# Kernel tuning notes

Hardware: AMD Instinct MI355X
Metric: run time of the kernel (lower is better)

## Reference

```python
import jax, jax.numpy as jnp
import numpy as np

NUM_LABELS = 64  # number of distinct label ids (0 = background, unchanged)


def setup_inputs() -> dict:
    key = jax.random.key(0)
    k1, k2, k3 = jax.random.split(key, 3)
    shape = (2, 192, 256, 256)
    texturized = jax.random.normal(k1, shape, dtype=jnp.float32)
    label_map = jax.random.randint(k2, shape, 0, NUM_LABELS, dtype=jnp.int32)
    # one Uniform(0, intensity) draw per label, mirroring self.intensity() per loop iter
    intensities = jax.random.uniform(k3, (NUM_LABELS,), dtype=jnp.float32)
    return {"texturized": texturized, "label_map": label_map, "intensities": intensities}


def reference(texturized, label_map, intensities):
    # Per label l > 0 (torch loop): adjusted[mask_l] -= mean(tex[mask_l] - intensity_l)
    #                             = tex - (segment_mean_l - intensity_l) on mask_l.
    flat_tex = texturized.reshape(-1)
    flat_lab = label_map.reshape(-1)
    sums = jax.ops.segment_sum(flat_tex, flat_lab, num_segments=NUM_LABELS)
    counts = jax.ops.segment_sum(jnp.ones_like(flat_tex), flat_lab, num_segments=NUM_LABELS)
    means = sums / jnp.maximum(counts, 1.0)
    delta = means - intensities  # [NUM_LABELS] per-label bls.mean()
    adj = flat_tex - jnp.where(flat_lab > 0, delta[flat_lab], 0.0)
    return adj.reshape(texturized.shape)
```

## Files before the change

### kernel.cpp

```cpp
#include <hip/hip_runtime.h>

#define NL 64

__global__ __launch_bounds__(64) void tl_reduce(const float* __restrict__ tex,
                                                const int* __restrict__ lab,
                                                float* __restrict__ g_sums,
                                                float* __restrict__ g_cnts,
                                                int n) {
    __shared__ float s_sum[NL][NL];
    __shared__ float s_cnt[NL][NL];
    const int lane = threadIdx.x;

    float4 z = make_float4(0.f, 0.f, 0.f, 0.f);
    float4* ps = (float4*)&s_sum[0][0];
    float4* pc = (float4*)&s_cnt[0][0];
    #pragma unroll
    for (int i = 0; i < (NL * NL / 4) / NL; ++i) {
        ps[i * NL + lane] = z;
        pc[i * NL + lane] = z;
    }
    __syncthreads();

    const int n4 = n >> 2;
    const float4* __restrict__ tex4 = (const float4*)tex;
    const int4* __restrict__ lab4 = (const int4*)lab;
    const int stride = gridDim.x * NL;

    int i = blockIdx.x * NL + lane;
    bool valid = i < n4;
    float4 t; int4 l;
    if (valid) { t = tex4[i]; l = lab4[i]; }
    while (valid) {
        const int inext = i + stride;
        const bool vnext = inext < n4;
        float4 tn; int4 ln;
        if (vnext) { tn = tex4[inext]; ln = lab4[inext]; }

        s_sum[l.x & (NL - 1)][lane] += t.x;  s_cnt[l.x & (NL - 1)][lane] += 1.0f;
        s_sum[l.y & (NL - 1)][lane] += t.y;  s_cnt[l.y & (NL - 1)][lane] += 1.0f;
        s_sum[l.z & (NL - 1)][lane] += t.z;  s_cnt[l.z & (NL - 1)][lane] += 1.0f;
        s_sum[l.w & (NL - 1)][lane] += t.w;  s_cnt[l.w & (NL - 1)][lane] += 1.0f;

        i = inext; valid = vnext; t = tn; l = ln;
    }

    if (blockIdx.x == 0) {
        const int base = n4 << 2;
        const int rem = n - base;
        if (lane < rem) {
            const int j = base + lane;
            s_sum[lab[j] & (NL - 1)][lane] += tex[j];
            s_cnt[lab[j] & (NL - 1)][lane] += 1.0f;
        }
    }
    __syncthreads();

    float s = 0.f, c = 0.f;
    #pragma unroll
    for (int k = 0; k < NL; ++k) {
        const int col = (k + lane) & (NL - 1);
        s += s_sum[lane][col];
        c += s_cnt[lane][col];
    }
    atomicAdd(&g_sums[lane], s);
    atomicAdd(&g_cnts[lane], c);
}

__global__ __launch_bounds__(256) void tl_apply(const float* __restrict__ tex,
                                                const int* __restrict__ lab,
                                                const float* __restrict__ g_sums,
                                                const float* __restrict__ g_cnts,
                                                const float* __restrict__ intens,
                                                float* __restrict__ out, int n) {
    __shared__ float s_delta[NL];
    if (threadIdx.x < NL) {
        const int l = threadIdx.x;
        const float mean = g_sums[l] / fmaxf(g_cnts[l], 1.0f);
        s_delta[l] = (l > 0) ? (mean - intens[l]) : 0.0f;
    }
    __syncthreads();

    const int n4 = n >> 2;
    const int i = blockIdx.x * blockDim.x + threadIdx.x;
    if (i < n4) {
        const float4 t = ((const float4*)tex)[i];
        const int4 l = ((const int4*)lab)[i];
        float4 o;
        o.x = t.x - s_delta[l.x & (NL - 1)];
        o.y = t.y - s_delta[l.y & (NL - 1)];
        o.z = t.z - s_delta[l.z & (NL - 1)];
        o.w = t.w - s_delta[l.w & (NL - 1)];
        ((float4*)out)[i] = o;
    }
    if (blockIdx.x == 0) {
        const int base = n4 << 2;
        const int rem = n - base;
        if ((int)threadIdx.x < rem) {
            const int j = base + threadIdx.x;
            out[j] = tex[j] - s_delta[lab[j] & (NL - 1)];
        }
    }
}

extern "C" void kernel_launch(void* const* d_in, const int* in_sizes, int n_in,
                              void* d_out, int out_size, void* d_ws, size_t ws_size,
                              hipStream_t stream) {
    const float* tex    = (const float*)d_in[0];
    const int*   lab    = (const int*)d_in[1];
    const float* intens = (const float*)d_in[2];
    float* out = (float*)d_out;
    const int n = in_sizes[0];

    float* g_sums = (float*)d_ws;
    float* g_cnts = (float*)((char*)d_ws + NL * sizeof(float));

    hipMemsetAsync(d_ws, 0, 2 * NL * sizeof(float), stream);

    tl_reduce<<<1280, NL, 0, stream>>>(tex, lab, g_sums, g_cnts, n);

    const int n4 = n >> 2;
    const int blocks = (n4 + 255) / 256;
    tl_apply<<<blocks, 256, 0, stream>>>(tex, lab, g_sums, g_cnts, intens, out, n);
}
```

Before: 354.0 us.

## Use 256-thread reduce blocks with shared atomics and packed 16-bit counts

The per-label reduction kernel moves from 64-thread blocks with a private per-lane histogram column to 256-thread blocks, where four wavefronts share each column through LDS atomics. Counts are packed as two 16-bit halves per word and kept as unsigned integers, which halves count storage and leaves room for the larger blocks. The final reduction splits the 64 columns across four wavefronts and combines their partials before the global atomics, and the grid grows to 1536 blocks. This aims for more resident waves and better latency hiding. The cost is LDS atomic contention, and the 16-bit counts could overflow if one lane column saw more than 65535 elements of a label per block.

New measurement: 338.0 us. -4.5%, faster.

```diff
diff --git a/kernel.cpp b/kernel.cpp
--- a/kernel.cpp
+++ b/kernel.cpp
@@ -2,80 +2,109 @@
 
 #define NL 64
 
-__global__ __launch_bounds__(64) void tl_reduce(const float* __restrict__ tex,
-                                                const int* __restrict__ lab,
-                                                float* __restrict__ g_sums,
-                                                float* __restrict__ g_cnts,
-                                                int n) {
-    __shared__ float s_sum[NL][NL];
-    __shared__ float s_cnt[NL][NL];
-    const int lane = threadIdx.x;
+__global__ __launch_bounds__(256) void tl_reduce(const float* __restrict__ tex,
+                                                 const int* __restrict__ lab,
+                                                 float* __restrict__ g_sums,
+                                                 unsigned int* __restrict__ g_cnts,
+                                                 int n) {
+    __shared__ float s_sum[NL * NL];
+    __shared__ unsigned int s_cnt[(NL / 2) * NL];
+    __shared__ float s_part[256];
+    __shared__ float c_part[256];
 
-    float4 z = make_float4(0.f, 0.f, 0.f, 0.f);
-    float4* ps = (float4*)&s_sum[0][0];
-    float4* pc = (float4*)&s_cnt[0][0];
-    #pragma unroll
-    for (int i = 0; i < (NL * NL / 4) / NL; ++i) {
-        ps[i * NL + lane] = z;
-        pc[i * NL + lane] = z;
-    }
+    const int tid = threadIdx.x;
+    const int col = tid & (NL - 1);
+
+    for (int i = tid; i < NL * NL; i += 256) s_sum[i] = 0.0f;
+    for (int i = tid; i < (NL / 2) * NL; i += 256) s_cnt[i] = 0u;
     __syncthreads();
 
     const int n4 = n >> 2;
     const float4* __restrict__ tex4 = (const float4*)tex;
     const int4* __restrict__ lab4 = (const int4*)lab;
-    const int stride = gridDim.x * NL;
+    const int stride = gridDim.x * 256;
 
-    int i = blockIdx.x * NL + lane;
-    bool valid = i < n4;
+    int i = blockIdx.x * 256 + tid;
+    bool v = i < n4;
     float4 t; int4 l;
-    if (valid) { t = tex4[i]; l = lab4[i]; }
-    while (valid) {
+    if (v) { t = tex4[i]; l = lab4[i]; }
+    while (v) {
         const int inext = i + stride;
-        const bool vnext = inext < n4;
+        const bool vn = inext < n4;
         float4 tn; int4 ln;
-        if (vnext) { tn = tex4[inext]; ln = lab4[inext]; }
+        if (vn) { tn = tex4[inext]; ln = lab4[inext]; }
 
-        s_sum[l.x & (NL - 1)][lane] += t.x;  s_cnt[l.x & (NL - 1)][lane] += 1.0f;
-        s_sum[l.y & (NL - 1)][lane] += t.y;  s_cnt[l.y & (NL - 1)][lane] += 1.0f;
-        s_sum[l.z & (NL - 1)][lane] += t.z;  s_cnt[l.z & (NL - 1)][lane] += 1.0f;
-        s_sum[l.w & (NL - 1)][lane] += t.w;  s_cnt[l.w & (NL - 1)][lane] += 1.0f;
+        {
+            const int lb = l.x & (NL - 1);
+            atomicAdd(&s_sum[(lb << 6) | col], t.x);
+            atomicAdd(&s_cnt[((lb >> 1) << 6) | col], 1u << ((lb & 1) << 4));
+        }
+        {
+            const int lb = l.y & (NL - 1);
+            atomicAdd(&s_sum[(lb << 6) | col], t.y);
+            atomicAdd(&s_cnt[((lb >> 1) << 6) | col], 1u << ((lb & 1) << 4));
+        }
+        {
+            const int lb = l.z & (NL - 1);
+            atomicAdd(&s_sum[(lb << 6) | col], t.z);
+            atomicAdd(&s_cnt[((lb >> 1) << 6) | col], 1u << ((lb & 1) << 4));
+        }
+        {
+            const int lb = l.w & (NL - 1);
+            atomicAdd(&s_sum[(lb << 6) | col], t.w);
+            atomicAdd(&s_cnt[((lb >> 1) << 6) | col], 1u << ((lb & 1) << 4));
+        }
 
-        i = inext; valid = vnext; t = tn; l = ln;
+        i = inext; v = vn; t = tn; l = ln;
     }
 
     if (blockIdx.x == 0) {
         const int base = n4 << 2;
         const int rem = n - base;
-        if (lane < rem) {
-            const int j = base + lane;
-            s_sum[lab[j] & (NL - 1)][lane] += tex[j];
-            s_cnt[lab[j] & (NL - 1)][lane] += 1.0f;
+        if (tid < rem) {
+            const int j = base + tid;
+            const int lb = lab[j] & (NL - 1);
+            atomicAdd(&s_sum[(lb << 6) | col], tex[j]);
+            atomicAdd(&s_cnt[((lb >> 1) << 6) | col], 1u << ((lb & 1) << 4));
         }
     }
     __syncthreads();
 
-    float s = 0.f, c = 0.f;
-    #pragma unroll
-    for (int k = 0; k < NL; ++k) {
-        const int col = (k + lane) & (NL - 1);
-        s += s_sum[lane][col];
-        c += s_cnt[lane][col];
+    {
+        const int label = tid & (NL - 1);
+        const int w = tid >> 6;
+        float s = 0.0f;
+        unsigned int c = 0u;
+        const int sh = (label & 1) << 4;
+        #pragma unroll
+        for (int k = 0; k < 16; ++k) {
+            const int cc = (w << 4) | ((k + tid) & 15);
+            s += s_sum[(label << 6) | cc];
+            c += (s_cnt[((label >> 1) << 6) | cc] >> sh) & 0xffffu;
+        }
+        s_part[tid] = s;
+        c_part[tid] = (float)c;
     }
-    atomicAdd(&g_sums[lane], s);
-    atomicAdd(&g_cnts[lane], c);
+    __syncthreads();
+
+    if (tid < NL) {
+        const float ss = s_part[tid] + s_part[64 + tid] + s_part[128 + tid] + s_part[192 + tid];
+        const float cc = c_part[tid] + c_part[64 + tid] + c_part[128 + tid] + c_part[192 + tid];
+        atomicAdd(&g_sums[tid], ss);
+        atomicAdd(&g_cnts[tid], (unsigned int)cc);
+    }
 }
 
 __global__ __launch_bounds__(256) void tl_apply(const float* __restrict__ tex,
                                                 const int* __restrict__ lab,
                                                 const float* __restrict__ g_sums,
-                                                const float* __restrict__ g_cnts,
+                                                const unsigned int* __restrict__ g_cnts,
                                                 const float* __restrict__ intens,
                                                 float* __restrict__ out, int n) {
     __shared__ float s_delta[NL];
     if (threadIdx.x < NL) {
         const int l = threadIdx.x;
-        const float mean = g_sums[l] / fmaxf(g_cnts[l], 1.0f);
+        const float mean = g_sums[l] / fmaxf((float)g_cnts[l], 1.0f);
         s_delta[l] = (l > 0) ? (mean - intens[l]) : 0.0f;
     }
     __syncthreads();
@@ -112,11 +141,11 @@
     const int n = in_sizes[0];
 
     float* g_sums = (float*)d_ws;
-    float* g_cnts = (float*)((char*)d_ws + NL * sizeof(float));
+    unsigned int* g_cnts = (unsigned int*)((char*)d_ws + NL * sizeof(float));
 
     hipMemsetAsync(d_ws, 0, 2 * NL * sizeof(float), stream);
 
-    tl_reduce<<<1280, NL, 0, stream>>>(tex, lab, g_sums, g_cnts, n);
+    tl_reduce<<<1536, 256, 0, stream>>>(tex, lab, g_sums, g_cnts, n);
 
     const int n4 = n >> 2;
     const int blocks = (n4 + 255) / 256;
```
